# Performance work log

Measured on AMD Instinct MI355X. Metric: run time of the kernel, lower is better.

## Reference

```python
import jax, jax.numpy as jnp
import numpy as np

B, T, D = 4, 2048, 1024
N_HEAD, HEAD_SIZE = 16, 64
MASK_FILL = 1e-9  # faithful to original: masked_fill uses 1e-9, not -inf


def setup_inputs() -> dict:
    key = jax.random.key(0)
    k1, k2, k3 = jax.random.split(key, 3)
    x = jax.random.normal(k1, (B, T, D), dtype=jnp.float32)
    # per-head qkv projection weights, stacked: [n_head, d_model, 3*head_size]
    W_qkv = jax.random.normal(k2, (N_HEAD, D, 3 * HEAD_SIZE), dtype=jnp.float32) * (D ** -0.5)
    # output projection [d_model, d_model] (x @ W_out convention)
    W_out = jax.random.normal(k3, (D, D), dtype=jnp.float32) * (D ** -0.5)
    return {"x": x, "W_qkv": W_qkv, "W_out": W_out}


def reference(x, W_qkv, W_out):
    Bv, Tv, C = x.shape
    # qkv for all heads at once: [B, H, T, 3*head_size]
    qkv = jnp.einsum("btc,hcf->bhtf", x, W_qkv)
    q, k, v = jnp.split(qkv, 3, axis=-1)  # each [B, H, T, head_size]
    # NOTE: original scales by C**-0.5 where C = d_model (not head_size)
    scores = jnp.einsum("bhtd,bhsd->bhts", q, k) * (C ** -0.5)
    causal = jnp.tril(jnp.ones((Tv, Tv), dtype=bool))
    # faithful bug: masked positions set to 1e-9 before softmax (not -inf)
    scores = jnp.where(causal, scores, MASK_FILL)
    attn = jax.nn.softmax(scores, axis=-1)
    out_heads = jnp.einsum("bhts,bhsd->bhtd", attn, v)  # [B, H, T, head_size]
    mha = out_heads.transpose(0, 2, 1, 3).reshape(Bv, Tv, C)  # concat heads
    return mha @ W_out
```

## Files before the change

kernel.cpp:

```cpp
#include <hip/hip_runtime.h>

typedef unsigned short u16;
typedef __attribute__((ext_vector_type(8))) short short8;
typedef __attribute__((ext_vector_type(4))) short short4v;
typedef __attribute__((ext_vector_type(4))) float f32x4;

#define B_  4
#define T_  2048
#define D_  1024
#define H_  16
#define HS_ 64
#define M_    (B_ * T_)
#define NQKV_ (H_ * 3 * HS_)
#define NTILE_ (T_ / 64)
#define LOG2E_ 1.44269504088896340736f

__device__ __forceinline__ u16 f2bf(float f) {
  union { float f; unsigned u; } v; v.f = f;
  unsigned u = v.u;
  return (u16)((u + 0x7FFFu + ((u >> 16) & 1u)) >> 16);
}
__device__ __forceinline__ float bf2f(u16 h) {
  union { unsigned u; float f; } v; v.u = ((unsigned)h) << 16; return v.f;
}
__device__ __forceinline__ unsigned pkbf(float lo, float hi) {
  unsigned r;
  asm("v_cvt_pk_bf16_f32 %0, %1, %2" : "=v"(r) : "v"(lo), "v"(hi));
  return r;
}
__device__ __forceinline__ float exp2fast(float x) {
  float r;
  asm("v_exp_f32 %0, %1" : "=v"(r) : "v"(x));
  return r;
}
__device__ __forceinline__ void gload16(const u16* g, u16* l) {
  __builtin_amdgcn_global_load_lds(
      (const __attribute__((address_space(1))) void*)g,
      (__attribute__((address_space(3))) void*)l, 16, 0, 0);
}

__global__ void k_cvt_x(const float* __restrict__ x, u16* __restrict__ o, int n4) {
  int i = blockIdx.x * 256 + threadIdx.x;
  if (i < n4) {
    float4 v = ((const float4*)x)[i];
    short4v d;
    d[0] = (short)f2bf(v.x); d[1] = (short)f2bf(v.y);
    d[2] = (short)f2bf(v.z); d[3] = (short)f2bf(v.w);
    ((short4v*)o)[i] = d;
  }
}

__global__ void k_transpose_cvt(const float* __restrict__ in, u16* __restrict__ out,
                                int R, int C, long sIn, long sOut) {
  __shared__ float tile[32][33];
  int h = blockIdx.z;
  const float* src = in + (long)h * sIn;
  u16* dst = out + (long)h * sOut;
  int r0 = blockIdx.y * 32, c0 = blockIdx.x * 32;
  int tx = threadIdx.x, ty = threadIdx.y;
  #pragma unroll
  for (int i = 0; i < 32; i += 8) {
    int r = r0 + ty + i, c = c0 + tx;
    tile[ty + i][tx] = (r < R && c < C) ? src[(long)r * C + c] : 0.f;
  }
  __syncthreads();
  #pragma unroll
  for (int i = 0; i < 32; i += 8) {
    int c = c0 + ty + i, r = r0 + tx;
    if (c < C && r < R) dst[(long)c * R + r] = f2bf(tile[tx][ty + i]);
  }
}

template<int MODE>
__global__ __launch_bounds__(256) void k_gemm(
    const u16* __restrict__ A, const u16* __restrict__ Bt,
    u16* __restrict__ Oq, u16* __restrict__ Ok, u16* __restrict__ Ov,
    float* __restrict__ Of, int K) {
  __shared__ __align__(16) u16 smem[128 * 128];
  u16* As = smem;
  u16* Bs = smem + 128 * 64;
  int mt = blockIdx.x, nt = blockIdx.y;
  int tid = threadIdx.x;
  int wid = tid >> 6, lane = tid & 63;
  int lr = lane & 15, lg = lane >> 4;
  int mw = (wid >> 1) * 64, nw = (wid & 1) * 64;
  const u16* srcA[4]; const u16* srcB[4];
  u16* dstA[4]; u16* dstB[4];
  #pragma unroll
  for (int l = 0; l < 4; l++) {
    int c = l * 256 + wid * 64 + lane;
    int r = c >> 3, q = c & 7;
    int qs = q ^ (r & 7);
    srcA[l] = A  + (long)(mt * 128 + r) * K + qs * 8;
    srcB[l] = Bt + (long)(nt * 128 + r) * K + qs * 8;
    dstA[l] = As + (l * 256 + wid * 64) * 8;
    dstB[l] = Bs + (l * 256 + wid * 64) * 8;
  }
  const int rsw = (lr & 7);
  f32x4 acc[4][4] = {};
  for (int k0 = 0; k0 < K; k0 += 64) {
    __syncthreads();
    #pragma unroll
    for (int l = 0; l < 4; l++) gload16(srcA[l] + k0, dstA[l]);
    #pragma unroll
    for (int l = 0; l < 4; l++) gload16(srcB[l] + k0, dstB[l]);
    __syncthreads();
    #pragma unroll
    for (int kk = 0; kk < 2; kk++) {
      short8 af[4], bf[4];
      #pragma unroll
      for (int i = 0; i < 4; i++)
        af[i] = *(const short8*)(As + (mw + i * 16 + lr) * 64 + (((kk * 4 + lg) ^ rsw) << 3));
      #pragma unroll
      for (int i = 0; i < 4; i++)
        bf[i] = *(const short8*)(Bs + (nw + i * 16 + lr) * 64 + (((kk * 4 + lg) ^ rsw) << 3));
      #pragma unroll
      for (int i = 0; i < 4; i++)
        #pragma unroll
        for (int j = 0; j < 4; j++)
          acc[i][j] = __builtin_amdgcn_mfma_f32_16x16x32_bf16(af[i], bf[j], acc[i][j], 0, 0, 0);
    }
  }
  __syncthreads();
  if constexpr (MODE == 0) {
    u16* Cs = smem;
    #pragma unroll
    for (int j = 0; j < 4; j++) {
      int fbase = (nt * 128 + nw + j * 16) % 192;
      float sc = (fbase < 64) ? (0.03125f * LOG2E_) : 1.0f;
      #pragma unroll
      for (int i = 0; i < 4; i++) {
        int row = mw + i * 16 + lg * 4;
        int col = nw + j * 16 + lr;
        #pragma unroll
        for (int r = 0; r < 4; r++)
          Cs[(row + r) * 128 + col] = f2bf(acc[i][j][r] * sc);
      }
    }
    __syncthreads();
    #pragma unroll
    for (int p5 = 0; p5 < 8; p5++) {
      int idx = p5 * 2048 + tid * 8;
      int row = idx >> 7, col = idx & 127;
      short8 v = *(const short8*)(Cs + row * 128 + col);
      int m = mt * 128 + row;
      int n0 = nt * 128 + col;
      int b = m >> 11, t = m & (T_ - 1);
      int h = n0 / 192, f = n0 % 192;
      long o = (((long)(b * H_ + h)) * T_ + t) * HS_;
      u16* dst = (f < 64) ? (Oq + o + f) : (f < 128) ? (Ok + o + f - 64) : (Ov + o + f - 128);
      *(short8*)dst = v;
    }
  } else {
    #pragma unroll
    for (int i = 0; i < 4; i++) {
      #pragma unroll
      for (int j = 0; j < 4; j++) {
        int mbase = mt * 128 + mw + i * 16 + lg * 4;
        int n     = nt * 128 + nw + j * 16 + lr;
        #pragma unroll
        for (int r = 0; r < 4; r++)
          Of[(long)(mbase + r) * D_ + n] = acc[i][j][r];
      }
    }
  }
}

__global__ void k_transpose_v(const u16* __restrict__ V, u16* __restrict__ Vp,
                              float* __restrict__ Partial) {
  __shared__ u16 tile[64][65];
  __shared__ float psum[4][64];
  int bh = blockIdx.z;
  int jt = blockIdx.x;
  int t0 = jt * 64;
  int tx = threadIdx.x & 63, ty = threadIdx.x >> 6;
  const u16* src = V + (long)bh * T_ * HS_;
  u16* dtile = Vp + (((long)bh * NTILE_) + jt) * 64 * 64;
  #pragma unroll
  for (int i = 0; i < 64; i += 4)
    tile[ty + i][tx] = src[(long)(t0 + ty + i) * HS_ + tx];
  __syncthreads();
  int pos = ((tx >> 2) & 3) * 16 + ((tx >> 4) & 3) * 4 + (tx & 3);
  #pragma unroll
  for (int i = 0; i < 64; i += 4)
    dtile[(ty + i) * 64 + pos] = tile[tx][ty + i];
  float s = 0.f;
  #pragma unroll
  for (int i = 0; i < 16; i++)
    s += bf2f(tile[ty * 16 + i][tx]);
  psum[ty][tx] = s;
  __syncthreads();
  if (threadIdx.x < 64)
    Partial[((long)bh * NTILE_ + jt) * HS_ + threadIdx.x] =
        psum[0][threadIdx.x] + psum[1][threadIdx.x] + psum[2][threadIdx.x] + psum[3][threadIdx.x];
}

__global__ void k_vscan(const float* __restrict__ Partial, float* __restrict__ Suf) {
  int bh = blockIdx.x;
  int d = threadIdx.x;
  const float* Pb = Partial + (long)bh * NTILE_ * HS_;
  float* Sb = Suf + (long)bh * (NTILE_ + 1) * HS_;
  float acc = 0.f;
  Sb[NTILE_ * HS_ + d] = 0.f;
  for (int j = NTILE_ - 1; j >= 0; j--) {
    acc += Pb[j * HS_ + d];
    Sb[j * HS_ + d] = acc;
  }
}

__global__ __launch_bounds__(512, 2) void k_attn(
    const u16* __restrict__ Q, const u16* __restrict__ Kc,
    const u16* __restrict__ Vp, const float* __restrict__ Suf,
    u16* __restrict__ Mha) {
  __shared__ __align__(16) u16 Ks[2][64 * 64];
  __shared__ __align__(16) u16 Vs[2][64 * 64];
  int bh = blockIdx.x;
  int st = 7 - (int)blockIdx.y;
  int b = bh >> 4, h = bh & 15;
  int tid = threadIdx.x, wid = tid >> 6, lane = tid & 63;
  int lr = lane & 15, lg = lane >> 4;
  const u16* Qb = Q  + (long)bh * T_ * HS_;
  const u16* Kb = Kc + (long)bh * T_ * HS_;
  const u16* Vb = Vp + (long)bh * T_ * HS_;
  union U8 { unsigned u[4]; short8 s; };
  const short8 vone = { (short)0x3F80, (short)0x3F80, (short)0x3F80, (short)0x3F80,
                        (short)0x3F80, (short)0x3F80, (short)0x3F80, (short)0x3F80 };
  int srow = tid >> 3;
  int schunk = (tid & 7) ^ (srow & 7);
  const u16* kSrc = Kb + srow * 64 + schunk * 8;
  const u16* vSrc = Vb + srow * 64 + schunk * 8;
  const int r7 = lr & 7;
  const int kc0 = (lg ^ r7) << 3, kc1 = ((4 + lg) ^ r7) << 3;
  const int vc0 = ((2 * lg) ^ r7) << 3, vc1 = ((2 * lg + 1) ^ r7) << 3;

  int q0w = st * 256 + wid * 32;
  short8 qf[2][2];
  #pragma unroll
  for (int g = 0; g < 2; g++) {
    const u16* qp = Qb + (long)(q0w + g * 16 + lr) * HS_;
    qf[g][0] = *(const short8*)(qp + lg * 8);
    qf[g][1] = *(const short8*)(qp + 32 + lg * 8);
  }
  f32x4 accO[2][4] = {};
  f32x4 accL[2] = {};
  const int blkJ = 4 * st + 3;
  const int myJ  = 4 * st + (wid >> 1);
  gload16(kSrc, &Ks[0][wid * 512]);
  gload16(vSrc, &Vs[0][wid * 512]);
  __syncthreads();
  for (int jt = 0; jt <= blkJ; jt++) {
    int cur = jt & 1;
    if (jt < blkJ) {
      long off = (long)(jt + 1) * 4096;
      gload16(kSrc + off, &Ks[cur ^ 1][wid * 512]);
      gload16(vSrc + off, &Vs[cur ^ 1][wid * 512]);
    }
    if (jt <= myJ) {
      int j0 = jt * 64;
      const bool diag = (jt == myJ);
      const u16* Kl = Ks[cur];
      const u16* Vl = Vs[cur];
      f32x4 s4[2][4];
      #pragma unroll
      for (int fn = 0; fn < 4; fn++) {
        const u16* krow = Kl + (fn * 16 + lr) * 64;
        short8 kb0 = *(const short8*)(krow + kc0);
        short8 kb1 = *(const short8*)(krow + kc1);
        #pragma unroll
        for (int g = 0; g < 2; g++) {
          f32x4 z = {};
          z = __builtin_amdgcn_mfma_f32_16x16x32_bf16(kb0, qf[g][0], z, 0, 0, 0);
          z = __builtin_amdgcn_mfma_f32_16x16x32_bf16(kb1, qf[g][1], z, 0, 0, 0);
          s4[g][fn] = z;
        }
      }
      U8 pa[2][2];
      #pragma unroll
      for (int g = 0; g < 2; g++) {
        int qrow = q0w + g * 16 + lr;
        float p[4][4];
        #pragma unroll
        for (int fn = 0; fn < 4; fn++) {
          #pragma unroll
          for (int r = 0; r < 4; r++) {
            float v = s4[g][fn][r];
            if (diag) {
              int s = j0 + fn * 16 + lg * 4 + r;
              v = (s <= qrow) ? v : 0.0f;
            }
            p[fn][r] = exp2fast(v);
          }
        }
        pa[g][0].u[0] = pkbf(p[0][0], p[0][1]); pa[g][0].u[1] = pkbf(p[0][2], p[0][3]);
        pa[g][0].u[2] = pkbf(p[1][0], p[1][1]); pa[g][0].u[3] = pkbf(p[1][2], p[1][3]);
        pa[g][1].u[0] = pkbf(p[2][0], p[2][1]); pa[g][1].u[1] = pkbf(p[2][2], p[2][3]);
        pa[g][1].u[2] = pkbf(p[3][0], p[3][1]); pa[g][1].u[3] = pkbf(p[3][2], p[3][3]);
        accL[g] = __builtin_amdgcn_mfma_f32_16x16x32_bf16(pa[g][0].s, vone, accL[g], 0, 0, 0);
        accL[g] = __builtin_amdgcn_mfma_f32_16x16x32_bf16(pa[g][1].s, vone, accL[g], 0, 0, 0);
      }
      #pragma unroll
      for (int fd = 0; fd < 4; fd++) {
        const u16* vrow = Vl + (fd * 16 + lr) * 64;
        U8 vb0, vb1;
        vb0.s = *(const short8*)(vrow + vc0);
        vb1.s = *(const short8*)(vrow + vc1);
        #pragma unroll
        for (int g = 0; g < 2; g++) {
          accO[g][fd] = __builtin_amdgcn_mfma_f32_16x16x32_bf16(pa[g][0].s, vb0.s, accO[g][fd], 0, 0, 0);
          accO[g][fd] = __builtin_amdgcn_mfma_f32_16x16x32_bf16(pa[g][1].s, vb1.s, accO[g][fd], 0, 0, 0);
        }
      }
    }
    __syncthreads();
  }
  int nmask = T_ - (myJ + 1) * 64;
  const float* sufp = Suf + ((long)bh * (NTILE_ + 1) + (myJ + 1)) * HS_;
  float sufv[4];
  #pragma unroll
  for (int fd = 0; fd < 4; fd++) sufv[fd] = sufp[fd * 16 + lr];
  #pragma unroll
  for (int g = 0; g < 2; g++) {
    #pragma unroll
    for (int fd = 0; fd < 4; fd++) {
      #pragma unroll
      for (int r = 0; r < 4; r++) {
        int trow = q0w + g * 16 + lg * 4 + r;
        float o = (accO[g][fd][r] + sufv[fd]) / (accL[g][r] + (float)nmask);
        Mha[((long)(b * T_ + trow)) * D_ + h * HS_ + fd * 16 + lr] = f2bf(o);
      }
    }
  }
}

extern "C" void kernel_launch(void* const* d_in, const int* in_sizes, int n_in,
                              void* d_out, int out_size, void* d_ws, size_t ws_size,
                              hipStream_t stream) {
  const float* x    = (const float*)d_in[0];
  const float* wqkv = (const float*)d_in[1];
  const float* wout = (const float*)d_in[2];
  float* out = (float*)d_out;

  char* p = (char*)d_ws;
  u16* Xb    = (u16*)p; p += (size_t)M_ * D_ * 2;
  u16* WqkvT = (u16*)p; p += (size_t)NQKV_ * D_ * 2;
  u16* WoutT = (u16*)p; p += (size_t)D_ * D_ * 2;
  u16* Qw  = (u16*)p; p += (size_t)B_ * H_ * T_ * HS_ * 2;
  u16* Kw  = (u16*)p; p += (size_t)B_ * H_ * T_ * HS_ * 2;
  u16* Vw  = (u16*)p; p += (size_t)B_ * H_ * T_ * HS_ * 2;
  u16* Vpw = (u16*)p; p += (size_t)B_ * H_ * T_ * HS_ * 2;
  u16* Mha = (u16*)p; p += (size_t)M_ * D_ * 2;
  float* Suf = (float*)p; p += (size_t)B_ * H_ * (NTILE_ + 1) * HS_ * 4;
  float* Part = (float*)p; p += (size_t)B_ * H_ * NTILE_ * HS_ * 4;

  k_cvt_x<<<dim3(M_ * D_ / 4 / 256), dim3(256), 0, stream>>>(x, Xb, M_ * D_ / 4);
  k_transpose_cvt<<<dim3(192 / 32, D_ / 32, H_), dim3(32, 8), 0, stream>>>(
      wqkv, WqkvT, D_, 192, (long)D_ * 192, (long)192 * D_);
  k_transpose_cvt<<<dim3(D_ / 32, D_ / 32, 1), dim3(32, 8), 0, stream>>>(
      wout, WoutT, D_, D_, 0, 0);
  k_gemm<0><<<dim3(M_ / 128, NQKV_ / 128), dim3(256), 0, stream>>>(
      Xb, WqkvT, Qw, Kw, Vw, nullptr, D_);
  k_transpose_v<<<dim3(T_ / 64, 1, B_ * H_), dim3(256), 0, stream>>>(Vw, Vpw, Part);
  k_vscan<<<dim3(B_ * H_), dim3(64), 0, stream>>>(Part, Suf);
  k_attn<<<dim3(B_ * H_, 8), dim3(512), 0, stream>>>(Qw, Kw, Vpw, Suf, Mha);
  k_gemm<1><<<dim3(M_ / 128, D_ / 128), dim3(256), 0, stream>>>(
      Mha, WoutT, nullptr, nullptr, nullptr, out, D_);
}
```

Measured before the change: 167.8 us.

## Double-buffer GEMM LDS tiles with K-step 32 to overlap loads and MFMA

The GEMM main loop changes from a single 64-wide K tile, with two barriers per step, to double-buffered 32-wide K tiles. The next tile is prefetched into the alternate LDS buffer while MFMAs run on the current one, and each step needs only one barrier. The swizzle is adapted to 4 chunks per row. Each iteration now does half the MFMA work, so loop and barrier overhead rises relative to compute.

```diff
diff --git a/kernel.cpp b/kernel.cpp
--- a/kernel.cpp
+++ b/kernel.cpp
@@ -76,52 +76,57 @@
     const u16* __restrict__ A, const u16* __restrict__ Bt,
     u16* __restrict__ Oq, u16* __restrict__ Ok, u16* __restrict__ Ov,
     float* __restrict__ Of, int K) {
-  __shared__ __align__(16) u16 smem[128 * 128];
-  u16* As = smem;
-  u16* Bs = smem + 128 * 64;
+  __shared__ __align__(16) u16 smem[16384];
   int mt = blockIdx.x, nt = blockIdx.y;
   int tid = threadIdx.x;
   int wid = tid >> 6, lane = tid & 63;
   int lr = lane & 15, lg = lane >> 4;
   int mw = (wid >> 1) * 64, nw = (wid & 1) * 64;
-  const u16* srcA[4]; const u16* srcB[4];
-  u16* dstA[4]; u16* dstB[4];
-  #pragma unroll
-  for (int l = 0; l < 4; l++) {
-    int c = l * 256 + wid * 64 + lane;
-    int r = c >> 3, q = c & 7;
-    int qs = q ^ (r & 7);
-    srcA[l] = A  + (long)(mt * 128 + r) * K + qs * 8;
-    srcB[l] = Bt + (long)(nt * 128 + r) * K + qs * 8;
-    dstA[l] = As + (l * 256 + wid * 64) * 8;
-    dstB[l] = Bs + (l * 256 + wid * 64) * 8;
-  }
-  const int rsw = (lr & 7);
+  int c0 = wid * 128 + lane;
+  int r0 = c0 >> 2, q0 = (c0 & 3) ^ (r0 & 3);
+  int c1 = c0 + 64;
+  int r1 = c1 >> 2, q1 = (c1 & 3) ^ (r1 & 3);
+  const u16* srcA0 = A  + (long)(mt * 128 + r0) * K + q0 * 8;
+  const u16* srcA1 = A  + (long)(mt * 128 + r1) * K + q1 * 8;
+  const u16* srcB0 = Bt + (long)(nt * 128 + r0) * K + q0 * 8;
+  const u16* srcB1 = Bt + (long)(nt * 128 + r1) * K + q1 * 8;
+  const int wbase = (wid * 128) * 8;
+  const int rsw = lr & 3;
+  const int fcol = (lg ^ rsw) << 3;
   f32x4 acc[4][4] = {};
-  for (int k0 = 0; k0 < K; k0 += 64) {
+  const int nIter = K / 32;
+  gload16(srcA0, smem + wbase);
+  gload16(srcA1, smem + wbase + 512);
+  gload16(srcB0, smem + 8192 + wbase);
+  gload16(srcB1, smem + 8192 + wbase + 512);
+  __syncthreads();
+  for (int t = 0; t < nIter; t++) {
+    int cur = t & 1;
+    if (t + 1 < nIter) {
+      int k0 = (t + 1) * 32;
+      u16* a = smem + (cur ^ 1) * 4096 + wbase;
+      gload16(srcA0 + k0, a);
+      gload16(srcA1 + k0, a + 512);
+      u16* bb = smem + 8192 + (cur ^ 1) * 4096 + wbase;
+      gload16(srcB0 + k0, bb);
+      gload16(srcB1 + k0, bb + 512);
+    }
+    const u16* As = smem + cur * 4096;
+    const u16* Bs = smem + 8192 + cur * 4096;
+    short8 af[4], bf[4];
+    #pragma unroll
+    for (int i = 0; i < 4; i++)
+      af[i] = *(const short8*)(As + (mw + i * 16 + lr) * 32 + fcol);
+    #pragma unroll
+    for (int i = 0; i < 4; i++)
+      bf[i] = *(const short8*)(Bs + (nw + i * 16 + lr) * 32 + fcol);
+    #pragma unroll
+    for (int i = 0; i < 4; i++)
+      #pragma unroll
+      for (int j = 0; j < 4; j++)
+        acc[i][j] = __builtin_amdgcn_mfma_f32_16x16x32_bf16(af[i], bf[j], acc[i][j], 0, 0, 0);
     __syncthreads();
-    #pragma unroll
-    for (int l = 0; l < 4; l++) gload16(srcA[l] + k0, dstA[l]);
-    #pragma unroll
-    for (int l = 0; l < 4; l++) gload16(srcB[l] + k0, dstB[l]);
-    __syncthreads();
-    #pragma unroll
-    for (int kk = 0; kk < 2; kk++) {
-      short8 af[4], bf[4];
-      #pragma unroll
-      for (int i = 0; i < 4; i++)
-        af[i] = *(const short8*)(As + (mw + i * 16 + lr) * 64 + (((kk * 4 + lg) ^ rsw) << 3));
-      #pragma unroll
-      for (int i = 0; i < 4; i++)
-        bf[i] = *(const short8*)(Bs + (nw + i * 16 + lr) * 64 + (((kk * 4 + lg) ^ rsw) << 3));
-      #pragma unroll
-      for (int i = 0; i < 4; i++)
-        #pragma unroll
-        for (int j = 0; j < 4; j++)
-          acc[i][j] = __builtin_amdgcn_mfma_f32_16x16x32_bf16(af[i], bf[j], acc[i][j], 0, 0, 0);
-    }
-  }
-  __syncthreads();
+  }
   if constexpr (MODE == 0) {
     u16* Cs = smem;
     #pragma unroll
```

Result: no change. 168.9 us (+0.7%).

## Enlarge GEMM tiles to 256x256 with 8 waves and double-buffered LDS

Applied to the files above, without the earlier changes.

Both GEMMs (the QKV projection and the output projection) move from 128x128 tiles with 4 waves to 256x256 tiles with 8 waves per block. Each wave now holds 8x4 MFMA accumulators. LDS grows to 128KB for double buffering, and the next K-tile's global loads are issued before the current tile's MFMAs. The aim is more data reuse per load and overlap of memory with compute, but it raises register pressure, limits occupancy to one block per CU, and the output-projection GEMM launches only 128 blocks.

```diff
diff --git a/kernel.cpp b/kernel.cpp
--- a/kernel.cpp
+++ b/kernel.cpp
@@ -72,79 +72,90 @@
 }
 
 template<int MODE>
-__global__ __launch_bounds__(256) void k_gemm(
+__global__ __launch_bounds__(512) void k_gemm(
     const u16* __restrict__ A, const u16* __restrict__ Bt,
     u16* __restrict__ Oq, u16* __restrict__ Ok, u16* __restrict__ Ov,
     float* __restrict__ Of, int K) {
-  __shared__ __align__(16) u16 smem[128 * 128];
-  u16* As = smem;
-  u16* Bs = smem + 128 * 64;
+  __shared__ __align__(16) u16 smem[65536];
   int mt = blockIdx.x, nt = blockIdx.y;
   int tid = threadIdx.x;
   int wid = tid >> 6, lane = tid & 63;
   int lr = lane & 15, lg = lane >> 4;
-  int mw = (wid >> 1) * 64, nw = (wid & 1) * 64;
-  const u16* srcA[4]; const u16* srcB[4];
-  u16* dstA[4]; u16* dstB[4];
-  #pragma unroll
-  for (int l = 0; l < 4; l++) {
-    int c = l * 256 + wid * 64 + lane;
-    int r = c >> 3, q = c & 7;
-    int qs = q ^ (r & 7);
-    srcA[l] = A  + (long)(mt * 128 + r) * K + qs * 8;
-    srcB[l] = Bt + (long)(nt * 128 + r) * K + qs * 8;
-    dstA[l] = As + (l * 256 + wid * 64) * 8;
-    dstB[l] = Bs + (l * 256 + wid * 64) * 8;
-  }
-  const int rsw = (lr & 7);
-  f32x4 acc[4][4] = {};
-  for (int k0 = 0; k0 < K; k0 += 64) {
+  int wm = wid >> 2, wn = wid & 3;
+  const int rsw = lr & 7;
+  int r0c = tid >> 3,         q0c = (tid & 7) ^ (r0c & 7);
+  int r1c = (tid + 512) >> 3, q1c = ((tid + 512) & 7) ^ (r1c & 7);
+  const u16* gA = A  + (long)(mt * 256) * K;
+  const u16* gB = Bt + (long)(nt * 256) * K;
+  const u16* sA00 = gA + (long)r0c * K + q0c * 8;
+  const u16* sA01 = gA + (long)r1c * K + q1c * 8;
+  const u16* sA10 = gA + (long)(128 + r0c) * K + q0c * 8;
+  const u16* sA11 = gA + (long)(128 + r1c) * K + q1c * 8;
+  const u16* sB00 = gB + (long)r0c * K + q0c * 8;
+  const u16* sB01 = gB + (long)r1c * K + q1c * 8;
+  const u16* sB10 = gB + (long)(128 + r0c) * K + q0c * 8;
+  const u16* sB11 = gB + (long)(128 + r1c) * K + q1c * 8;
+  const int dst0 = (wid * 64) * 8;
+  const int dst1 = (wid * 64 + 512) * 8;
+
+#define STAGE_KT(bb, t) do { long ko = (long)(t) * 64;                       \
+    u16* d = smem + (bb) * 32768;                                            \
+    gload16(sA00 + ko, d + dst0);          gload16(sA01 + ko, d + dst1);     \
+    gload16(sA10 + ko, d + 8192 + dst0);   gload16(sA11 + ko, d + 8192 + dst1); \
+    gload16(sB00 + ko, d + 16384 + dst0);  gload16(sB01 + ko, d + 16384 + dst1); \
+    gload16(sB10 + ko, d + 24576 + dst0);  gload16(sB11 + ko, d + 24576 + dst1); } while (0)
+
+  f32x4 acc[8][4] = {};
+  const int nKT = K / 64;
+  STAGE_KT(0, 0);
+  __syncthreads();
+  for (int kt = 0; kt < nKT; kt++) {
+    int cur = kt & 1;
+    if (kt + 1 < nKT) STAGE_KT(cur ^ 1, kt + 1);
+    const u16* aB = smem + cur * 32768 + wm * 8192;
+    const u16* bB = smem + cur * 32768 + 16384 + (wn >> 1) * 8192;
+    #pragma unroll
+    for (int kk = 0; kk < 2; kk++) {
+      const int fc = ((kk * 4 + lg) ^ rsw) << 3;
+      short8 bf[4];
+      #pragma unroll
+      for (int fn = 0; fn < 4; fn++)
+        bf[fn] = *(const short8*)(bB + ((wn & 1) * 64 + fn * 16 + lr) * 64 + fc);
+      #pragma unroll
+      for (int fm = 0; fm < 8; fm++) {
+        short8 af = *(const short8*)(aB + (fm * 16 + lr) * 64 + fc);
+        #pragma unroll
+        for (int fn = 0; fn < 4; fn++)
+          acc[fm][fn] = __builtin_amdgcn_mfma_f32_16x16x32_bf16(af, bf[fn], acc[fm][fn], 0, 0, 0);
+      }
+    }
     __syncthreads();
-    #pragma unroll
-    for (int l = 0; l < 4; l++) gload16(srcA[l] + k0, dstA[l]);
-    #pragma unroll
-    for (int l = 0; l < 4; l++) gload16(srcB[l] + k0, dstB[l]);
-    __syncthreads();
-    #pragma unroll
-    for (int kk = 0; kk < 2; kk++) {
-      short8 af[4], bf[4];
-      #pragma unroll
-      for (int i = 0; i < 4; i++)
-        af[i] = *(const short8*)(As + (mw + i * 16 + lr) * 64 + (((kk * 4 + lg) ^ rsw) << 3));
-      #pragma unroll
-      for (int i = 0; i < 4; i++)
-        bf[i] = *(const short8*)(Bs + (nw + i * 16 + lr) * 64 + (((kk * 4 + lg) ^ rsw) << 3));
-      #pragma unroll
-      for (int i = 0; i < 4; i++)
-        #pragma unroll
-        for (int j = 0; j < 4; j++)
-          acc[i][j] = __builtin_amdgcn_mfma_f32_16x16x32_bf16(af[i], bf[j], acc[i][j], 0, 0, 0);
-    }
-  }
-  __syncthreads();
+  }
+#undef STAGE_KT
+
   if constexpr (MODE == 0) {
     u16* Cs = smem;
     #pragma unroll
-    for (int j = 0; j < 4; j++) {
-      int fbase = (nt * 128 + nw + j * 16) % 192;
+    for (int fn = 0; fn < 4; fn++) {
+      int fbase = (nt * 256 + wn * 64 + fn * 16) % 192;
       float sc = (fbase < 64) ? (0.03125f * LOG2E_) : 1.0f;
       #pragma unroll
-      for (int i = 0; i < 4; i++) {
-        int row = mw + i * 16 + lg * 4;
-        int col = nw + j * 16 + lr;
+      for (int fm = 0; fm < 8; fm++) {
+        int row = wm * 128 + fm * 16 + lg * 4;
+        int col = wn * 64 + fn * 16 + lr;
         #pragma unroll
         for (int r = 0; r < 4; r++)
-          Cs[(row + r) * 128 + col] = f2bf(acc[i][j][r] * sc);
+          Cs[(row + r) * 256 + col] = f2bf(acc[fm][fn][r] * sc);
       }
     }
     __syncthreads();
     #pragma unroll
-    for (int p5 = 0; p5 < 8; p5++) {
-      int idx = p5 * 2048 + tid * 8;
-      int row = idx >> 7, col = idx & 127;
-      short8 v = *(const short8*)(Cs + row * 128 + col);
-      int m = mt * 128 + row;
-      int n0 = nt * 128 + col;
+    for (int p5 = 0; p5 < 16; p5++) {
+      int idx = p5 * 4096 + tid * 8;
+      int row = idx >> 8, col = idx & 255;
+      short8 v = *(const short8*)(Cs + row * 256 + col);
+      int m = mt * 256 + row;
+      int n0 = nt * 256 + col;
       int b = m >> 11, t = m & (T_ - 1);
       int h = n0 / 192, f = n0 % 192;
       long o = (((long)(b * H_ + h)) * T_ + t) * HS_;
@@ -153,14 +164,14 @@
     }
   } else {
     #pragma unroll
-    for (int i = 0; i < 4; i++) {
-      #pragma unroll
-      for (int j = 0; j < 4; j++) {
-        int mbase = mt * 128 + mw + i * 16 + lg * 4;
-        int n     = nt * 128 + nw + j * 16 + lr;
+    for (int fm = 0; fm < 8; fm++) {
+      #pragma unroll
+      for (int fn = 0; fn < 4; fn++) {
+        int mbase = mt * 256 + wm * 128 + fm * 16 + lg * 4;
+        int n     = nt * 256 + wn * 64 + fn * 16 + lr;
         #pragma unroll
         for (int r = 0; r < 4; r++)
-          Of[(long)(mbase + r) * D_ + n] = acc[i][j][r];
+          Of[(long)(mbase + r) * D_ + n] = acc[fm][fn][r];
       }
     }
   }
@@ -357,11 +368,11 @@
       wqkv, WqkvT, D_, 192, (long)D_ * 192, (long)192 * D_);
   k_transpose_cvt<<<dim3(D_ / 32, D_ / 32, 1), dim3(32, 8), 0, stream>>>(
       wout, WoutT, D_, D_, 0, 0);
-  k_gemm<0><<<dim3(M_ / 128, NQKV_ / 128), dim3(256), 0, stream>>>(
+  k_gemm<0><<<dim3(M_ / 256, NQKV_ / 256), dim3(512), 0, stream>>>(
       Xb, WqkvT, Qw, Kw, Vw, nullptr, D_);
   k_transpose_v<<<dim3(T_ / 64, 1, B_ * H_), dim3(256), 0, stream>>>(Vw, Vpw, Part);
   k_vscan<<<dim3(B_ * H_), dim3(64), 0, stream>>>(Part, Suf);
   k_attn<<<dim3(B_ * H_, 8), dim3(512), 0, stream>>>(Qw, Kw, Vpw, Suf, Mha);
-  k_gemm<1><<<dim3(M_ / 128, D_ / 128), dim3(256), 0, stream>>>(
+  k_gemm<1><<<dim3(M_ / 256, D_ / 256), dim3(512), 0, stream>>>(
       Mha, WoutT, nullptr, nullptr, nullptr, out, D_);
 }
```

New measurement: 173.8 us. 1.04x slower.

## Double-buffer GEMM shared-memory tiles to overlap global loads with MFMA

Applied to the files above, without the earlier changes.

The GEMM kernel now uses two LDS buffers (64KB total), prefetching the next K tile into the alternate buffer while MFMAs consume the current one. This removes one barrier per iteration and is meant to hide global-to-LDS load latency behind compute. The cost is doubled LDS usage, which may reduce occupancy. The synchronization relies on gload16 completing before the barrier.

```diff
diff --git a/kernel.cpp b/kernel.cpp
--- a/kernel.cpp
+++ b/kernel.cpp
@@ -76,16 +76,14 @@
     const u16* __restrict__ A, const u16* __restrict__ Bt,
     u16* __restrict__ Oq, u16* __restrict__ Ok, u16* __restrict__ Ov,
     float* __restrict__ Of, int K) {
-  __shared__ __align__(16) u16 smem[128 * 128];
-  u16* As = smem;
-  u16* Bs = smem + 128 * 64;
+  __shared__ __align__(16) u16 smem[32768];
   int mt = blockIdx.x, nt = blockIdx.y;
   int tid = threadIdx.x;
   int wid = tid >> 6, lane = tid & 63;
   int lr = lane & 15, lg = lane >> 4;
   int mw = (wid >> 1) * 64, nw = (wid & 1) * 64;
   const u16* srcA[4]; const u16* srcB[4];
-  u16* dstA[4]; u16* dstB[4];
+  int dstOff[4];
   #pragma unroll
   for (int l = 0; l < 4; l++) {
     int c = l * 256 + wid * 64 + lane;
@@ -93,35 +91,51 @@
     int qs = q ^ (r & 7);
     srcA[l] = A  + (long)(mt * 128 + r) * K + qs * 8;
     srcB[l] = Bt + (long)(nt * 128 + r) * K + qs * 8;
-    dstA[l] = As + (l * 256 + wid * 64) * 8;
-    dstB[l] = Bs + (l * 256 + wid * 64) * 8;
+    dstOff[l] = (l * 256 + wid * 64) * 8;
   }
   const int rsw = (lr & 7);
   f32x4 acc[4][4] = {};
-  for (int k0 = 0; k0 < K; k0 += 64) {
-    __syncthreads();
-    #pragma unroll
-    for (int l = 0; l < 4; l++) gload16(srcA[l] + k0, dstA[l]);
-    #pragma unroll
-    for (int l = 0; l < 4; l++) gload16(srcB[l] + k0, dstB[l]);
-    __syncthreads();
+  const int nIter = K / 64;
+
+#define STAGE_G(bb, k0) do {                       \
+    u16* ab_ = smem + (bb) * 16384;                \
+    gload16(srcA[0] + (k0), ab_ + dstOff[0]);      \
+    gload16(srcA[1] + (k0), ab_ + dstOff[1]);      \
+    gload16(srcA[2] + (k0), ab_ + dstOff[2]);      \
+    gload16(srcA[3] + (k0), ab_ + dstOff[3]);      \
+    u16* bb_ = ab_ + 8192;                         \
+    gload16(srcB[0] + (k0), bb_ + dstOff[0]);      \
+    gload16(srcB[1] + (k0), bb_ + dstOff[1]);      \
+    gload16(srcB[2] + (k0), bb_ + dstOff[2]);      \
+    gload16(srcB[3] + (k0), bb_ + dstOff[3]); } while (0)
+
+  STAGE_G(0, 0);
+  __syncthreads();
+  for (int t = 0; t < nIter; t++) {
+    int cur = t & 1;
+    if (t + 1 < nIter) STAGE_G(cur ^ 1, (t + 1) * 64);
+    const u16* As = smem + cur * 16384;
+    const u16* Bs = As + 8192;
     #pragma unroll
     for (int kk = 0; kk < 2; kk++) {
+      const int fc = ((kk * 4 + lg) ^ rsw) << 3;
       short8 af[4], bf[4];
       #pragma unroll
       for (int i = 0; i < 4; i++)
-        af[i] = *(const short8*)(As + (mw + i * 16 + lr) * 64 + (((kk * 4 + lg) ^ rsw) << 3));
+        af[i] = *(const short8*)(As + (mw + i * 16 + lr) * 64 + fc);
       #pragma unroll
       for (int i = 0; i < 4; i++)
-        bf[i] = *(const short8*)(Bs + (nw + i * 16 + lr) * 64 + (((kk * 4 + lg) ^ rsw) << 3));
+        bf[i] = *(const short8*)(Bs + (nw + i * 16 + lr) * 64 + fc);
       #pragma unroll
       for (int i = 0; i < 4; i++)
         #pragma unroll
         for (int j = 0; j < 4; j++)
           acc[i][j] = __builtin_amdgcn_mfma_f32_16x16x32_bf16(af[i], bf[j], acc[i][j], 0, 0, 0);
     }
-  }
-  __syncthreads();
+    __syncthreads();
+  }
+#undef STAGE_G
+
   if constexpr (MODE == 0) {
     u16* Cs = smem;
     #pragma unroll
```

Result: faster. 159.4 us (-5.0%).
